# Optimization experiments

Hardware: AMD Instinct MI355X
Metric: run time of the kernel (lower is better)

Reference implementation:

```python
import jax, jax.numpy as jnp
import numpy as np

# Config constants (match init_kwargs)
E = 32          # num_experts
K = 4           # num_experts_per_token
G = 4           # num_expert_group
TG = 2          # topk_group
H = 2048        # hidden_size
F = 1024        # moe_intermediate_size
FS = 2048       # shared expert intermediate (moe_intermediate_size * num_shared_experts)
SCALE = 2.0     # routed_scaling_factor
B, S = 2, 1024
N = B * S
CAP = 2 * (N * K // E)


def setup_inputs() -> dict:
    key = jax.random.key(0)
    ks = jax.random.split(key, 9)
    w = 0.02  # init scale for weights
    return {
        "hidden_states": jax.random.normal(ks[0], (B, S, H), jnp.float32),
        "gate_w": jax.random.normal(ks[1], (E, H), jnp.float32) * w,
        "gate_bias": jax.random.normal(ks[2], (E,), jnp.float32) * w,
        "w1": jax.random.normal(ks[3], (E, H, F), jnp.float32) * w,
        "w2": jax.random.normal(ks[4], (E, F, H), jnp.float32) * w,
        "w3": jax.random.normal(ks[5], (E, H, F), jnp.float32) * w,
        "shared_gate": jax.random.normal(ks[6], (H, FS), jnp.float32) * w,
        "shared_up": jax.random.normal(ks[7], (H, FS), jnp.float32) * w,
        "shared_down": jax.random.normal(ks[8], (FS, H), jnp.float32) * w,
    }


def _gate(x, gate_w, gate_bias):
    # x: [N, H] -> (topk_idx [N,K] int32, topk_w [N,K] f32)
    logits = x @ gate_w.T                       # [N, E]
    scores = jax.nn.sigmoid(logits)
    sc = scores + gate_bias                     # scores_for_choice
    n = x.shape[0]
    grp = sc.reshape(n, G, E // G)
    group_scores = jax.lax.top_k(grp, 2)[0].sum(-1)          # [N, G]
    _, gidx = jax.lax.top_k(group_scores, TG)                # [N, TG]
    gmask = jnp.zeros((n, G), sc.dtype).at[jnp.arange(n)[:, None], gidx].set(1.0)
    smask = jnp.repeat(gmask, E // G, axis=1)                # [N, E]
    tmp = jnp.where(smask > 0, sc, 0.0)
    _, topk_idx = jax.lax.top_k(tmp, K)                      # [N, K]
    topk_w = jnp.take_along_axis(scores, topk_idx, axis=1)
    topk_w = topk_w / (topk_w.sum(-1, keepdims=True) + 1e-20)  # renormalize (K>1)
    return topk_idx, topk_w * SCALE


def _moe(x, topk_idx, topk_w, w1, w2, w3):
    # Capacity-based dispatch -> grouped SwiGLU GEMMs -> weighted combine.
    n = x.shape[0]
    flat_e = topk_idx.reshape(-1)                            # [N*K]
    oh = jax.nn.one_hot(flat_e, E, dtype=jnp.int32)
    pos = (jnp.cumsum(oh, axis=0) * oh).sum(-1) - 1          # slot within expert
    keep = pos < CAP
    slot = jnp.where(keep, pos, CAP)                         # CAP -> dropped via mode='drop'
    x_rep = jnp.repeat(x, K, axis=0)                         # [N*K, H]
    buf = jnp.zeros((E, CAP, H), x.dtype).at[flat_e, slot].set(x_rep, mode='drop')
    h = jax.nn.silu(jnp.einsum('ech,ehf->ecf', buf, w1)) * jnp.einsum('ech,ehf->ecf', buf, w3)
    ob = jnp.einsum('ecf,efh->ech', h, w2)                   # [E, CAP, H]
    y = ob[flat_e, jnp.minimum(slot, CAP - 1)]               # [N*K, H]
    y = jnp.where(keep[:, None], y, 0.0)
    return (y.reshape(n, K, H) * topk_w[:, :, None]).sum(1)  # [N, H]


def reference(hidden_states, gate_w, gate_bias, w1, w2, w3, shared_gate, shared_up, shared_down):
    b, s, h = hidden_states.shape
    x = hidden_states.reshape(-1, h)
    topk_idx, topk_w = _gate(x, gate_w, gate_bias)
    out = _moe(x, topk_idx, topk_w, w1, w2, w3)
    shared = (jax.nn.silu(x @ shared_gate) * (x @ shared_up)) @ shared_down
    return (out + shared).reshape(b, s, h)
```

## Files before the change

### kernel.cpp

```cpp
#include <hip/hip_runtime.h>
#include <stdint.h>
#include <math.h>

#define NTOK 2048
#define HDIM 2048
#define FDIM 1024
#define NEXP 32
#define TOPK 4
#define NGRP 4
#define CAP  512

typedef _Float16 f16;
typedef _Float16 half8 __attribute__((ext_vector_type(8)));
typedef float f32x4 __attribute__((ext_vector_type(4)));

__device__ __forceinline__ int swz3(int r) { return (r ^ (r >> 2)) & 3; }

__global__ __launch_bounds__(256) void convert_kernel(const float* __restrict__ x,
                                                      f16* __restrict__ xbt) {
  int i = blockIdx.x * 256 + threadIdx.x;
  int r = i >> 8;
  int c8 = (i & 255) << 3;
  const float* p = x + (size_t)r * HDIM + c8;
  f32x4 a = *(const f32x4*)p;
  f32x4 b = *(const f32x4*)(p + 4);
  half8 v;
  v[0] = (f16)a[0]; v[1] = (f16)a[1]; v[2] = (f16)a[2]; v[3] = (f16)a[3];
  v[4] = (f16)b[0]; v[5] = (f16)b[1]; v[6] = (f16)b[2]; v[7] = (f16)b[3];
  int t = c8 >> 5;
  *(half8*)((char*)xbt + (size_t)t * 131072 + r * 64 + (c8 & 31) * 2) = v;
}

__global__ __launch_bounds__(256) void gate_kernel(const float* __restrict__ x,
                                                   const float* __restrict__ gw,
                                                   const float* __restrict__ gb,
                                                   int* __restrict__ tidx,
                                                   float* __restrict__ tw) {
  int t = blockIdx.x;
  int tid = threadIdx.x;
  int e = tid >> 3, p = tid & 7;
  const f32x4* xr = (const f32x4*)(x + (size_t)t * HDIM);
  const f32x4* wr = (const f32x4*)(gw + (size_t)e * HDIM);
  float s = 0.f;
  for (int c = 0; c < 64; c++) {
    f32x4 a = xr[p + c * 8], w = wr[p + c * 8];
    s += a[0] * w[0] + a[1] * w[1] + a[2] * w[2] + a[3] * w[3];
  }
  s += __shfl_down(s, 4, 8);
  s += __shfl_down(s, 2, 8);
  s += __shfl_down(s, 1, 8);
  __shared__ float lg[NEXP];
  if (p == 0) lg[e] = s;
  __syncthreads();
  if (tid == 0) {
    float sc[NEXP], scb[NEXP];
    for (int i = 0; i < NEXP; i++) {
      sc[i] = 1.f / (1.f + expf(-lg[i]));
      scb[i] = sc[i] + gb[i];
    }
    float gs[NGRP];
    for (int g = 0; g < NGRP; g++) {
      float m1 = -1e30f, m2 = -1e30f;
      for (int j = 0; j < 8; j++) {
        float v = scb[g * 8 + j];
        if (v > m1) { m2 = m1; m1 = v; }
        else if (v > m2) m2 = v;
      }
      gs[g] = m1 + m2;
    }
    int g1 = 0; float bv = gs[0];
    for (int g = 1; g < NGRP; g++) if (gs[g] > bv) { bv = gs[g]; g1 = g; }
    int g2 = -1; bv = -1e30f;
    for (int g = 0; g < NGRP; g++) if (g != g1 && gs[g] > bv) { bv = gs[g]; g2 = g; }
    float cand[NEXP];
    for (int i = 0; i < NEXP; i++) {
      int g = i >> 3;
      cand[i] = (g == g1 || g == g2) ? scb[i] : 0.0f;
    }
    int isel[TOPK]; float wsel[TOPK]; float wsum = 0.f;
    bool used[NEXP] = {};
    for (int k = 0; k < TOPK; k++) {
      int best = 0; float bw = -1e30f;
      for (int i = 0; i < NEXP; i++)
        if (!used[i] && cand[i] > bw) { bw = cand[i]; best = i; }
      used[best] = true;
      isel[k] = best;
      wsel[k] = sc[best];
      wsum += wsel[k];
    }
    float inv = 2.0f / (wsum + 1e-20f);
    for (int k = 0; k < TOPK; k++) {
      tidx[t * TOPK + k] = isel[k];
      tw[t * TOPK + k] = wsel[k] * inv;
    }
  }
}

__global__ __launch_bounds__(256) void dispatch_kernel(const int* __restrict__ tidx,
                                                       const float* __restrict__ tw,
                                                       int* __restrict__ tok,
                                                       float* __restrict__ wt,
                                                       int* __restrict__ cnt) {
  int e = blockIdx.x, tid = threadIdx.x, wv = tid >> 6, lane = tid & 63;
  __shared__ int wsum[4];
  __shared__ int sbase;
  if (tid == 0) sbase = 0;
  __syncthreads();
  for (int c = 0; c < (NTOK * TOPK) / 256; c++) {
    int i = c * 256 + tid;
    int fe = tidx[i];
    bool flag = (fe == e);
    unsigned long long b = __ballot(flag ? 1 : 0);
    int lr = __popcll(b & ((1ull << lane) - 1ull));
    if (lane == 0) wsum[wv] = __popcll(b);
    __syncthreads();
    int off = 0;
    for (int w2 = 0; w2 < wv; w2++) off += wsum[w2];
    int tot = wsum[0] + wsum[1] + wsum[2] + wsum[3];
    int base = sbase;
    if (flag) {
      int pos = base + off + lr;
      if (pos < CAP) {
        tok[e * CAP + pos] = i >> 2;
        wt[e * CAP + pos] = tw[i];
      }
    }
    __syncthreads();
    if (tid == 0) sbase = base + tot;
  }
  __syncthreads();
  if (tid == 0) cnt[e] = min(sbase, CAP);
}

__global__ __launch_bounds__(256) void gather_kernel(const f16* __restrict__ xbt,
                                                     const int* __restrict__ tok,
                                                     const int* __restrict__ cnt,
                                                     f16* __restrict__ xg) {
  int bid = blockIdx.x;
  int t = bid & 63, e = bid >> 6;
  int cn = cnt[e];
  int tid = threadIdx.x;
  char* dst = (char*)xg + (size_t)e * 2097152 + (size_t)t * 32768;
  const char* srcb = (const char*)xbt + (size_t)t * 131072;
  for (int s = tid; s < CAP; s += 256) {
    uint4 v0 = {0,0,0,0}, v1 = {0,0,0,0}, v2 = {0,0,0,0}, v3 = {0,0,0,0};
    if (s < cn) {
      const uint4* sp = (const uint4*)(srcb + (size_t)tok[e * CAP + s] * 64);
      v0 = sp[0]; v1 = sp[1]; v2 = sp[2]; v3 = sp[3];
    }
    uint4* dp = (uint4*)(dst + s * 64);
    dp[0] = v0; dp[1] = v1; dp[2] = v2; dp[3] = v3;
  }
}

template<int MODE>
__global__ __launch_bounds__(256, (MODE == 1) ? 3 : ((MODE == 3) ? 4 : 2))
void gemm_kernel(const f16* __restrict__ Ag, const float* __restrict__ B0g,
                 const float* __restrict__ B1g, void* __restrict__ outp,
                 const int* __restrict__ tokL, const float* __restrict__ wtL,
                 const int* __restrict__ cntP) {
  constexpr int BM = (MODE == 0 || MODE == 2) ? 512 : 256;
  constexpr int BN = (MODE == 2) ? 64 : 32;
  constexpr bool DUAL = (MODE <= 1);
  constexpr int MF = BM / 64;
  constexpr int NF = BN / 16;
  constexpr int KD = (MODE == 2) ? 1024 : 2048;
  constexpr int NK = KD / 32;
  constexpr int ND = (MODE == 0) ? 1024 : 2048;
  constexpr int TS = (MODE == 0 || MODE == 2) ? 32768 : 131072;
  constexpr int BSZ = (DUAL ? 2 : 1) * BN * 64;

  int bid = blockIdx.x;
  int tid = threadIdx.x, lane = tid & 63, wv = tid >> 6;
  int e = 0, m0 = 0, n0 = 0;
  if constexpr (MODE == 0 || MODE == 2) {
    e = (bid & 7) + ((bid >> 3) >> 5) * 8;
    n0 = ((bid >> 3) & 31) * BN;
  } else {
    n0 = ((bid & 7) * 8 + ((bid >> 3) & 7)) * 32;
    m0 = ((bid >> 3) >> 3) * 256;
  }

  const char* Abase = (const char*)Ag;
  const float* B0 = B0g;
  const float* B1 = B1g;
  const int* tokp = tokL;
  const float* wtp = wtL;
  int Mcur = 0;
  if constexpr (MODE == 0 || MODE == 2) {
    Mcur = cntP[e];
    Abase += (size_t)e * ((MODE == 0) ? 2097152 : 1048576);
    B0 += (size_t)e * KD * ND;
    if constexpr (MODE == 0) B1 += (size_t)e * KD * ND;
    tokp += e * CAP;
    wtp += e * CAP;
  }

  __shared__ __align__(16) char bs[2 * BSZ];

  int kb = tid >> 3;
  int nbL = (tid & 7) * (BN / 8);

  unsigned voff[MF];
#pragma unroll
  for (int mf = 0; mf < MF; mf++) {
    int row = ((MODE == 0 || MODE == 2) ? (wv * (BM / 4)) : (m0 + wv * 64)) + mf * 16 + (lane & 15);
    voff[mf] = row * 64 + ((lane >> 4) << 4);
  }

  f32x4 acc0[MF][NF];
  f32x4 acc1[DUAL ? MF : 1][DUAL ? NF : 1];
#pragma unroll
  for (int mf = 0; mf < MF; mf++)
#pragma unroll
    for (int nf = 0; nf < NF; nf++) acc0[mf][nf] = (f32x4){0.f, 0.f, 0.f, 0.f};
  if constexpr (DUAL) {
#pragma unroll
    for (int mf = 0; mf < MF; mf++)
#pragma unroll
      for (int nf = 0; nf < NF; nf++) acc1[mf][nf] = (f32x4){0.f, 0.f, 0.f, 0.f};
  }

  half8 af[MF];
  half8 bf0[NF];
  half8 bf1[DUAL ? NF : 1];
  f32x4 bE0, bE1, bO0, bO1;

  auto loadB = [&](int t, f32x4& X, f32x4& Y) {
    const float* s = B0 + (size_t)(t * 32 + kb) * ND + n0 + nbL;
    X = *(const f32x4*)s;
    if constexpr (DUAL) {
      Y = *(const f32x4*)(B1 + (size_t)(t * 32 + kb) * ND + n0 + nbL);
    } else if constexpr (MODE == 2) {
      Y = *(const f32x4*)(s + 4);
    }
  };
  auto writeB = [&](const f32x4& X, const f32x4& Y, int par) {
    char* base = bs + par * BSZ;
#pragma unroll
    for (int q = 0; q < 4; q++) {
      int n = nbL + q;
      int off = n * 64 + (((kb >> 3) ^ swz3(n)) << 4) + (kb & 7) * 2;
      *(f16*)(base + off) = (f16)X[q];
      if constexpr (DUAL) {
        *(f16*)(base + BN * 64 + off) = (f16)Y[q];
      } else if constexpr (MODE == 2) {
        int n2 = n + 4;
        int off2 = n2 * 64 + (((kb >> 3) ^ swz3(n2)) << 4) + (kb & 7) * 2;
        *(f16*)(base + off2) = (f16)Y[q];
      }
    }
  };
  auto bfread = [&](int par) {
#pragma unroll
    for (int nf = 0; nf < NF; nf++) {
      int n = nf * 16 + (lane & 15);
      int off = par * BSZ + n * 64 + (((lane >> 4) ^ swz3(n)) << 4);
      bf0[nf] = *(const half8*)(bs + off);
      if constexpr (DUAL) bf1[nf] = *(const half8*)(bs + BN * 64 + off);
    }
  };
  auto loadAf = [&](int t) {
#pragma unroll
    for (int mf = 0; mf < MF; mf++)
      af[mf] = *(const half8*)(Abase + (size_t)t * TS + voff[mf]);
  };
  auto domfma = [&]() {
#pragma unroll
    for (int mf = 0; mf < MF; mf++)
#pragma unroll
      for (int nf = 0; nf < NF; nf++) {
        acc0[mf][nf] = __builtin_amdgcn_mfma_f32_16x16x32_f16(af[mf], bf0[nf], acc0[mf][nf], 0, 0, 0);
        if constexpr (DUAL)
          acc1[mf][nf] = __builtin_amdgcn_mfma_f32_16x16x32_f16(af[mf], bf1[nf], acc1[mf][nf], 0, 0, 0);
      }
  };

  loadB(0, bE0, bE1);
  loadB(1, bO0, bO1);
  loadAf(0);
  writeB(bE0, bE1, 0);
  asm volatile("s_waitcnt lgkmcnt(0)" ::: "memory");
  __builtin_amdgcn_s_barrier();

  for (int t = 0; t < NK; t += 2) {
    bfread(0);
    writeB(bO0, bO1, 1);
    if (t + 2 < NK) loadB(t + 2, bE0, bE1);
    domfma();
    loadAf(t + 1 < NK ? t + 1 : t);
    asm volatile("s_waitcnt lgkmcnt(0)" ::: "memory");
    __builtin_amdgcn_s_barrier();
    bfread(1);
    if (t + 2 < NK) writeB(bE0, bE1, 0);
    if (t + 3 < NK) loadB(t + 3, bO0, bO1);
    domfma();
    if (t + 2 < NK) {
      loadAf(t + 2);
      asm volatile("s_waitcnt lgkmcnt(0)" ::: "memory");
      __builtin_amdgcn_s_barrier();
    }
  }

  int koff = (lane >> 4) << 2;
  if constexpr (MODE == 0) {
    char* Hb = (char*)outp + (size_t)e * 1048576;
#pragma unroll
    for (int mf = 0; mf < MF; mf++)
#pragma unroll
      for (int j = 0; j < 4; j++) {
        int slot = wv * 128 + mf * 16 + koff + j;
#pragma unroll
        for (int nf = 0; nf < NF; nf++) {
          int col = n0 + nf * 16 + (lane & 15);
          float g = acc0[mf][nf][j], u = acc1[mf][nf][j];
          float val = g / (1.f + expf(-g)) * u;
          *(f16*)(Hb + (size_t)(col >> 5) * 32768 + slot * 64 + (col & 31) * 2) = (f16)val;
        }
      }
  } else if constexpr (MODE == 1) {
    char* Hb = (char*)outp;
#pragma unroll
    for (int mf = 0; mf < MF; mf++)
#pragma unroll
      for (int j = 0; j < 4; j++) {
        int row = m0 + wv * 64 + mf * 16 + koff + j;
#pragma unroll
        for (int nf = 0; nf < NF; nf++) {
          int col = n0 + nf * 16 + (lane & 15);
          float g = acc0[mf][nf][j], u = acc1[mf][nf][j];
          float val = g / (1.f + expf(-g)) * u;
          *(f16*)(Hb + (size_t)(col >> 5) * 131072 + row * 64 + (col & 31) * 2) = (f16)val;
        }
      }
  } else if constexpr (MODE == 2) {
    float* Of = (float*)outp;
#pragma unroll
    for (int mf = 0; mf < MF; mf++)
#pragma unroll
      for (int j = 0; j < 4; j++) {
        int slot = wv * 128 + mf * 16 + koff + j;
        if (slot < Mcur) {
          int tk = tokp[slot];
          float w = wtp[slot];
#pragma unroll
          for (int nf = 0; nf < NF; nf++) {
            int col = n0 + nf * 16 + (lane & 15);
            atomicAdd(Of + (size_t)tk * HDIM + col, acc0[mf][nf][j] * w);
          }
        }
      }
  } else {
    float* Of = (float*)outp;
#pragma unroll
    for (int mf = 0; mf < MF; mf++)
#pragma unroll
      for (int j = 0; j < 4; j++) {
        int row = m0 + wv * 64 + mf * 16 + koff + j;
#pragma unroll
        for (int nf = 0; nf < NF; nf++) {
          int col = n0 + nf * 16 + (lane & 15);
          Of[(size_t)row * HDIM + col] = acc0[mf][nf][j];
        }
      }
  }
}

extern "C" void kernel_launch(void* const* d_in, const int* in_sizes, int n_in,
                              void* d_out, int out_size, void* d_ws, size_t ws_size,
                              hipStream_t stream) {
  const float* x  = (const float*)d_in[0];
  const float* gw = (const float*)d_in[1];
  const float* gb = (const float*)d_in[2];
  const float* w1 = (const float*)d_in[3];
  const float* w2 = (const float*)d_in[4];
  const float* w3 = (const float*)d_in[5];
  const float* sg = (const float*)d_in[6];
  const float* su = (const float*)d_in[7];
  const float* sd = (const float*)d_in[8];
  float* out = (float*)d_out;
  char* ws = (char*)d_ws;

  f16*   xbt = (f16*)(ws);
  f16*   hs  = (f16*)(ws + 8388608);
  f16*   hbuf= (f16*)(ws + 16777216);
  f16*   xg  = (f16*)(ws + 50331648);
  int*   tok = (int*)(ws + 117440512);
  float* wt  = (float*)(ws + 117506048);
  int*   tidx= (int*)(ws + 117571584);
  float* tw  = (float*)(ws + 117604352);
  int*   cnt = (int*)(ws + 117637120);

  convert_kernel<<<2048, 256, 0, stream>>>(x, xbt);
  gate_kernel<<<2048, 256, 0, stream>>>(x, gw, gb, tidx, tw);
  dispatch_kernel<<<32, 256, 0, stream>>>(tidx, tw, tok, wt, cnt);
  gather_kernel<<<2048, 256, 0, stream>>>(xbt, tok, cnt, xg);

  gemm_kernel<0><<<1024, 256, 0, stream>>>(xg, w1, w3, hbuf, tok, wt, cnt);
  gemm_kernel<1><<<512, 256, 0, stream>>>(xbt, sg, su, hs, nullptr, nullptr, nullptr);
  gemm_kernel<3><<<512, 256, 0, stream>>>(hs, sd, nullptr, out, nullptr, nullptr, nullptr);
  gemm_kernel<2><<<1024, 256, 0, stream>>>(hbuf, w2, nullptr, out, tok, wt, cnt);
}
```

Before: 564.6 us.

## Load fp32 weights straight into MFMA B fragments, drop LDS staging

Each lane now loads B weights from global memory directly into registers, in the layout the MFMA fragment needs, and converts them to fp16 in registers. This removes the shared-memory staging, swizzle and barriers. Routed-expert blocks now skip waves whose rows are past the expert's token count. Tiling changes to BN=32 with one expert per block-index low bits, the mode-2 grid doubles, and the launch-bounds occupancy hints change. In exchange there are scalar, strided global loads that are less coalesced (16 columns across lanes, 8 rows per lane), and each wave re-reads B with no reuse across waves.

New measurement: 758.0 us. 34.2% more time.

```diff
diff --git a/kernel.cpp b/kernel.cpp
--- a/kernel.cpp
+++ b/kernel.cpp
@@ -13,8 +13,6 @@
 typedef _Float16 f16;
 typedef _Float16 half8 __attribute__((ext_vector_type(8)));
 typedef float f32x4 __attribute__((ext_vector_type(4)));
-
-__device__ __forceinline__ int swz3(int r) { return (r ^ (r >> 2)) & 3; }
 
 __global__ __launch_bounds__(256) void convert_kernel(const float* __restrict__ x,
                                                       f16* __restrict__ xbt) {
@@ -154,153 +152,125 @@
 }
 
 template<int MODE>
-__global__ __launch_bounds__(256, (MODE == 1) ? 3 : ((MODE == 3) ? 4 : 2))
+__global__ __launch_bounds__(256, (MODE <= 1) ? 2 : 3)
 void gemm_kernel(const f16* __restrict__ Ag, const float* __restrict__ B0g,
                  const float* __restrict__ B1g, void* __restrict__ outp,
                  const int* __restrict__ tokL, const float* __restrict__ wtL,
                  const int* __restrict__ cntP) {
-  constexpr int BM = (MODE == 0 || MODE == 2) ? 512 : 256;
-  constexpr int BN = (MODE == 2) ? 64 : 32;
   constexpr bool DUAL = (MODE <= 1);
-  constexpr int MF = BM / 64;
-  constexpr int NF = BN / 16;
+  constexpr bool ROUTED = (MODE == 0 || MODE == 2);
+  constexpr int WM = ROUTED ? 128 : 64;
+  constexpr int MF = WM / 16;
+  constexpr int NF = 2;
   constexpr int KD = (MODE == 2) ? 1024 : 2048;
   constexpr int NK = KD / 32;
   constexpr int ND = (MODE == 0) ? 1024 : 2048;
-  constexpr int TS = (MODE == 0 || MODE == 2) ? 32768 : 131072;
-  constexpr int BSZ = (DUAL ? 2 : 1) * BN * 64;
+  constexpr size_t TS = ROUTED ? 32768 : 131072;
 
   int bid = blockIdx.x;
   int tid = threadIdx.x, lane = tid & 63, wv = tid >> 6;
+
   int e = 0, m0 = 0, n0 = 0;
-  if constexpr (MODE == 0 || MODE == 2) {
-    e = (bid & 7) + ((bid >> 3) >> 5) * 8;
-    n0 = ((bid >> 3) & 31) * BN;
+  if constexpr (ROUTED) {
+    e = bid & 31;
+    n0 = (bid >> 5) * 32;
   } else {
-    n0 = ((bid & 7) * 8 + ((bid >> 3) & 7)) * 32;
-    m0 = ((bid >> 3) >> 3) * 256;
-  }
-
-  const char* Abase = (const char*)Ag;
+    m0 = (bid & 7) * 256;
+    n0 = (bid >> 3) * 32;
+  }
+
+  const char* Ab = (const char*)Ag;
   const float* B0 = B0g;
   const float* B1 = B1g;
-  const int* tokp = tokL;
-  const float* wtp = wtL;
-  int Mcur = 0;
-  if constexpr (MODE == 0 || MODE == 2) {
+  int Mcur = NTOK;
+  if constexpr (ROUTED) {
     Mcur = cntP[e];
-    Abase += (size_t)e * ((MODE == 0) ? 2097152 : 1048576);
-    B0 += (size_t)e * KD * ND;
-    if constexpr (MODE == 0) B1 += (size_t)e * KD * ND;
-    tokp += e * CAP;
-    wtp += e * CAP;
-  }
-
-  __shared__ __align__(16) char bs[2 * BSZ];
-
-  int kb = tid >> 3;
-  int nbL = (tid & 7) * (BN / 8);
-
-  unsigned voff[MF];
+    int Mpad = (Mcur + 127) & ~127;
+    if (wv * 128 >= Mpad) return;
+    Ab += (size_t)e * ((MODE == 0) ? 2097152 : 1048576);
+    B0 += (size_t)e * ((size_t)KD * ND);
+    if constexpr (DUAL) B1 += (size_t)e * ((size_t)KD * ND);
+  }
+
+  unsigned aoff[MF];
 #pragma unroll
   for (int mf = 0; mf < MF; mf++) {
-    int row = ((MODE == 0 || MODE == 2) ? (wv * (BM / 4)) : (m0 + wv * 64)) + mf * 16 + (lane & 15);
-    voff[mf] = row * 64 + ((lane >> 4) << 4);
-  }
-
+    int row = (ROUTED ? wv * WM : m0 + wv * WM) + mf * 16 + (lane & 15);
+    aoff[mf] = row * 64 + ((lane >> 4) << 4);
+  }
+
+  int q8 = (lane >> 4) * 8;
+  int nc = n0 + (lane & 15);
+
+  float bst0[NF][8];
+  float bst1[DUAL ? NF : 1][8];
+  half8 bc0[NF];
+  half8 bc1[DUAL ? NF : 1];
+  half8 afA[MF], afB[MF];
   f32x4 acc0[MF][NF];
   f32x4 acc1[DUAL ? MF : 1][DUAL ? NF : 1];
 #pragma unroll
   for (int mf = 0; mf < MF; mf++)
 #pragma unroll
-    for (int nf = 0; nf < NF; nf++) acc0[mf][nf] = (f32x4){0.f, 0.f, 0.f, 0.f};
+    for (int f = 0; f < NF; f++) acc0[mf][f] = (f32x4){0.f, 0.f, 0.f, 0.f};
   if constexpr (DUAL) {
 #pragma unroll
     for (int mf = 0; mf < MF; mf++)
 #pragma unroll
-      for (int nf = 0; nf < NF; nf++) acc1[mf][nf] = (f32x4){0.f, 0.f, 0.f, 0.f};
-  }
-
-  half8 af[MF];
-  half8 bf0[NF];
-  half8 bf1[DUAL ? NF : 1];
-  f32x4 bE0, bE1, bO0, bO1;
-
-  auto loadB = [&](int t, f32x4& X, f32x4& Y) {
-    const float* s = B0 + (size_t)(t * 32 + kb) * ND + n0 + nbL;
-    X = *(const f32x4*)s;
-    if constexpr (DUAL) {
-      Y = *(const f32x4*)(B1 + (size_t)(t * 32 + kb) * ND + n0 + nbL);
-    } else if constexpr (MODE == 2) {
-      Y = *(const f32x4*)(s + 4);
+      for (int f = 0; f < NF; f++) acc1[mf][f] = (f32x4){0.f, 0.f, 0.f, 0.f};
+  }
+
+  auto loadB = [&](int t) {
+#pragma unroll
+    for (int i = 0; i < 8; i++) {
+      size_t ro = (size_t)(t * 32 + q8 + i) * ND + nc;
+      bst0[0][i] = B0[ro];
+      bst0[1][i] = B0[ro + 16];
+      if constexpr (DUAL) {
+        bst1[0][i] = B1[ro];
+        bst1[1][i] = B1[ro + 16];
+      }
     }
   };
-  auto writeB = [&](const f32x4& X, const f32x4& Y, int par) {
-    char* base = bs + par * BSZ;
-#pragma unroll
-    for (int q = 0; q < 4; q++) {
-      int n = nbL + q;
-      int off = n * 64 + (((kb >> 3) ^ swz3(n)) << 4) + (kb & 7) * 2;
-      *(f16*)(base + off) = (f16)X[q];
-      if constexpr (DUAL) {
-        *(f16*)(base + BN * 64 + off) = (f16)Y[q];
-      } else if constexpr (MODE == 2) {
-        int n2 = n + 4;
-        int off2 = n2 * 64 + (((kb >> 3) ^ swz3(n2)) << 4) + (kb & 7) * 2;
-        *(f16*)(base + off2) = (f16)Y[q];
-      }
-    }
+  auto cvtB = [&]() {
+#pragma unroll
+    for (int f = 0; f < NF; f++)
+#pragma unroll
+      for (int i = 0; i < 8; i++) {
+        bc0[f][i] = (f16)bst0[f][i];
+        if constexpr (DUAL) bc1[f][i] = (f16)bst1[f][i];
+      }
   };
-  auto bfread = [&](int par) {
-#pragma unroll
-    for (int nf = 0; nf < NF; nf++) {
-      int n = nf * 16 + (lane & 15);
-      int off = par * BSZ + n * 64 + (((lane >> 4) ^ swz3(n)) << 4);
-      bf0[nf] = *(const half8*)(bs + off);
-      if constexpr (DUAL) bf1[nf] = *(const half8*)(bs + BN * 64 + off);
-    }
-  };
-  auto loadAf = [&](int t) {
-#pragma unroll
-    for (int mf = 0; mf < MF; mf++)
-      af[mf] = *(const half8*)(Abase + (size_t)t * TS + voff[mf]);
-  };
-  auto domfma = [&]() {
-#pragma unroll
-    for (int mf = 0; mf < MF; mf++)
-#pragma unroll
-      for (int nf = 0; nf < NF; nf++) {
-        acc0[mf][nf] = __builtin_amdgcn_mfma_f32_16x16x32_f16(af[mf], bf0[nf], acc0[mf][nf], 0, 0, 0);
-        if constexpr (DUAL)
-          acc1[mf][nf] = __builtin_amdgcn_mfma_f32_16x16x32_f16(af[mf], bf1[nf], acc1[mf][nf], 0, 0, 0);
-      }
-  };
-
-  loadB(0, bE0, bE1);
-  loadB(1, bO0, bO1);
-  loadAf(0);
-  writeB(bE0, bE1, 0);
-  asm volatile("s_waitcnt lgkmcnt(0)" ::: "memory");
-  __builtin_amdgcn_s_barrier();
-
+
+#define LOADAF(t, AF) { \
+  _Pragma("unroll") \
+  for (int mf = 0; mf < MF; mf++) \
+    AF[mf] = *(const half8*)(Ab + (size_t)(t) * TS + aoff[mf]); }
+
+#define DOMFMA(AF) { \
+  _Pragma("unroll") \
+  for (int mf = 0; mf < MF; mf++) { \
+    _Pragma("unroll") \
+    for (int f = 0; f < NF; f++) { \
+      acc0[mf][f] = __builtin_amdgcn_mfma_f32_16x16x32_f16(AF[mf], bc0[f], acc0[mf][f], 0, 0, 0); \
+      if constexpr (DUAL) \
+        acc1[mf][f] = __builtin_amdgcn_mfma_f32_16x16x32_f16(AF[mf], bc1[f], acc1[mf][f], 0, 0, 0); \
+    } } }
+
+  loadB(0);
+  LOADAF(0, afA)
   for (int t = 0; t < NK; t += 2) {
-    bfread(0);
-    writeB(bO0, bO1, 1);
-    if (t + 2 < NK) loadB(t + 2, bE0, bE1);
-    domfma();
-    loadAf(t + 1 < NK ? t + 1 : t);
-    asm volatile("s_waitcnt lgkmcnt(0)" ::: "memory");
-    __builtin_amdgcn_s_barrier();
-    bfread(1);
-    if (t + 2 < NK) writeB(bE0, bE1, 0);
-    if (t + 3 < NK) loadB(t + 3, bO0, bO1);
-    domfma();
-    if (t + 2 < NK) {
-      loadAf(t + 2);
-      asm volatile("s_waitcnt lgkmcnt(0)" ::: "memory");
-      __builtin_amdgcn_s_barrier();
-    }
-  }
+    cvtB();
+    loadB(t + 1);
+    DOMFMA(afA)
+    LOADAF(t + 1, afB)
+    cvtB();
+    if (t + 2 < NK) loadB(t + 2);
+    DOMFMA(afB)
+    if (t + 2 < NK) LOADAF(t + 2, afA)
+  }
+#undef LOADAF
+#undef DOMFMA
 
   int koff = (lane >> 4) << 2;
   if constexpr (MODE == 0) {
@@ -311,9 +281,9 @@
       for (int j = 0; j < 4; j++) {
         int slot = wv * 128 + mf * 16 + koff + j;
 #pragma unroll
-        for (int nf = 0; nf < NF; nf++) {
-          int col = n0 + nf * 16 + (lane & 15);
-          float g = acc0[mf][nf][j], u = acc1[mf][nf][j];
+        for (int f = 0; f < NF; f++) {
+          int col = n0 + f * 16 + (lane & 15);
+          float g = acc0[mf][f][j], u = acc1[mf][f][j];
           float val = g / (1.f + expf(-g)) * u;
           *(f16*)(Hb + (size_t)(col >> 5) * 32768 + slot * 64 + (col & 31) * 2) = (f16)val;
         }
@@ -326,15 +296,17 @@
       for (int j = 0; j < 4; j++) {
         int row = m0 + wv * 64 + mf * 16 + koff + j;
 #pragma unroll
-        for (int nf = 0; nf < NF; nf++) {
-          int col = n0 + nf * 16 + (lane & 15);
-          float g = acc0[mf][nf][j], u = acc1[mf][nf][j];
+        for (int f = 0; f < NF; f++) {
+          int col = n0 + f * 16 + (lane & 15);
+          float g = acc0[mf][f][j], u = acc1[mf][f][j];
           float val = g / (1.f + expf(-g)) * u;
           *(f16*)(Hb + (size_t)(col >> 5) * 131072 + row * 64 + (col & 31) * 2) = (f16)val;
         }
       }
   } else if constexpr (MODE == 2) {
     float* Of = (float*)outp;
+    const int* tokp = tokL + e * CAP;
+    const float* wtp = wtL + e * CAP;
 #pragma unroll
     for (int mf = 0; mf < MF; mf++)
 #pragma unroll
@@ -344,9 +316,9 @@
           int tk = tokp[slot];
           float w = wtp[slot];
 #pragma unroll
-          for (int nf = 0; nf < NF; nf++) {
-            int col = n0 + nf * 16 + (lane & 15);
-            atomicAdd(Of + (size_t)tk * HDIM + col, acc0[mf][nf][j] * w);
+          for (int f = 0; f < NF; f++) {
+            int col = n0 + f * 16 + (lane & 15);
+            atomicAdd(Of + (size_t)tk * HDIM + col, acc0[mf][f][j] * w);
           }
         }
       }
@@ -358,9 +330,9 @@
       for (int j = 0; j < 4; j++) {
         int row = m0 + wv * 64 + mf * 16 + koff + j;
 #pragma unroll
-        for (int nf = 0; nf < NF; nf++) {
-          int col = n0 + nf * 16 + (lane & 15);
-          Of[(size_t)row * HDIM + col] = acc0[mf][nf][j];
+        for (int f = 0; f < NF; f++) {
+          int col = n0 + f * 16 + (lane & 15);
+          Of[(size_t)row * HDIM + col] = acc0[mf][f][j];
         }
       }
   }
@@ -399,5 +371,5 @@
   gemm_kernel<0><<<1024, 256, 0, stream>>>(xg, w1, w3, hbuf, tok, wt, cnt);
   gemm_kernel<1><<<512, 256, 0, stream>>>(xbt, sg, su, hs, nullptr, nullptr, nullptr);
   gemm_kernel<3><<<512, 256, 0, stream>>>(hs, sd, nullptr, out, nullptr, nullptr, nullptr);
-  gemm_kernel<2><<<1024, 256, 0, stream>>>(hbuf, w2, nullptr, out, tok, wt, cnt);
-}
+  gemm_kernel<2><<<2048, 256, 0, stream>>>(hbuf, w2, nullptr, out, tok, wt, cnt);
+}
```

## Fuse routed and shared expert GEMMs into combined up and down launches

Applied to the files above, without the earlier changes.

The fp16 conversion of x now happens inside the gate kernel, so x is read once by one kernel instead of two. The gather now copies only occupied capacity slots and no longer zero-fills padding. The routed and shared up-projection GEMMs run as one launch, and the two down-projection GEMMs run as another, so the two expert paths can overlap on the device. Because both down GEMMs now add into the same output, the output is cleared with a memset and the shared path switches to atomic adds. The costs are extra atomic traffic on the output and lower allowed occupancy for the shared GEMM variants, since their launch bounds drop to 2 per CU.

Result: faster. 545.4 us (-3.4%).

```diff
diff --git a/kernel.cpp b/kernel.cpp
--- a/kernel.cpp
+++ b/kernel.cpp
@@ -14,28 +14,14 @@
 typedef _Float16 half8 __attribute__((ext_vector_type(8)));
 typedef float f32x4 __attribute__((ext_vector_type(4)));
 
-__device__ __forceinline__ int swz3(int r) { return (r ^ (r >> 2)) & 3; }
-
-__global__ __launch_bounds__(256) void convert_kernel(const float* __restrict__ x,
-                                                      f16* __restrict__ xbt) {
-  int i = blockIdx.x * 256 + threadIdx.x;
-  int r = i >> 8;
-  int c8 = (i & 255) << 3;
-  const float* p = x + (size_t)r * HDIM + c8;
-  f32x4 a = *(const f32x4*)p;
-  f32x4 b = *(const f32x4*)(p + 4);
-  half8 v;
-  v[0] = (f16)a[0]; v[1] = (f16)a[1]; v[2] = (f16)a[2]; v[3] = (f16)a[3];
-  v[4] = (f16)b[0]; v[5] = (f16)b[1]; v[6] = (f16)b[2]; v[7] = (f16)b[3];
-  int t = c8 >> 5;
-  *(half8*)((char*)xbt + (size_t)t * 131072 + r * 64 + (c8 & 31) * 2) = v;
-}
-
-__global__ __launch_bounds__(256) void gate_kernel(const float* __restrict__ x,
-                                                   const float* __restrict__ gw,
-                                                   const float* __restrict__ gb,
-                                                   int* __restrict__ tidx,
-                                                   float* __restrict__ tw) {
+__device__ __forceinline__ int swz3(int n) { return (n ^ (n >> 2)) & 3; }
+
+__global__ __launch_bounds__(256) void gateconv_kernel(const float* __restrict__ x,
+                                                       const float* __restrict__ gw,
+                                                       const float* __restrict__ gb,
+                                                       int* __restrict__ tidx,
+                                                       float* __restrict__ tw,
+                                                       f16* __restrict__ xbt) {
   int t = blockIdx.x;
   int tid = threadIdx.x;
   int e = tid >> 3, p = tid & 7;
@@ -51,6 +37,18 @@
   s += __shfl_down(s, 1, 8);
   __shared__ float lg[NEXP];
   if (p == 0) lg[e] = s;
+
+  {
+    int c8 = tid * 8;
+    const float* pp = x + (size_t)t * HDIM + c8;
+    f32x4 a = *(const f32x4*)pp;
+    f32x4 b = *(const f32x4*)(pp + 4);
+    half8 v;
+    v[0] = (f16)a[0]; v[1] = (f16)a[1]; v[2] = (f16)a[2]; v[3] = (f16)a[3];
+    v[4] = (f16)b[0]; v[5] = (f16)b[1]; v[6] = (f16)b[2]; v[7] = (f16)b[3];
+    *(half8*)((char*)xbt + (size_t)(c8 >> 5) * 131072 + t * 64 + (c8 & 31) * 2) = v;
+  }
+
   __syncthreads();
   if (tid == 0) {
     float sc[NEXP], scb[NEXP];
@@ -142,23 +140,19 @@
   int tid = threadIdx.x;
   char* dst = (char*)xg + (size_t)e * 2097152 + (size_t)t * 32768;
   const char* srcb = (const char*)xbt + (size_t)t * 131072;
-  for (int s = tid; s < CAP; s += 256) {
-    uint4 v0 = {0,0,0,0}, v1 = {0,0,0,0}, v2 = {0,0,0,0}, v3 = {0,0,0,0};
-    if (s < cn) {
-      const uint4* sp = (const uint4*)(srcb + (size_t)tok[e * CAP + s] * 64);
-      v0 = sp[0]; v1 = sp[1]; v2 = sp[2]; v3 = sp[3];
-    }
+  for (int s = tid; s < cn; s += 256) {
+    const uint4* sp = (const uint4*)(srcb + (size_t)tok[e * CAP + s] * 64);
+    uint4 v0 = sp[0], v1 = sp[1], v2 = sp[2], v3 = sp[3];
     uint4* dp = (uint4*)(dst + s * 64);
     dp[0] = v0; dp[1] = v1; dp[2] = v2; dp[3] = v3;
   }
 }
 
 template<int MODE>
-__global__ __launch_bounds__(256, (MODE == 1) ? 3 : ((MODE == 3) ? 4 : 2))
-void gemm_kernel(const f16* __restrict__ Ag, const float* __restrict__ B0g,
-                 const float* __restrict__ B1g, void* __restrict__ outp,
-                 const int* __restrict__ tokL, const float* __restrict__ wtL,
-                 const int* __restrict__ cntP) {
+__device__ void gemm_body(int bid, const f16* __restrict__ Ag, const float* __restrict__ B0g,
+                          const float* __restrict__ B1g, void* __restrict__ outp,
+                          const int* __restrict__ tokL, const float* __restrict__ wtL,
+                          const int* __restrict__ cntP, char* bs) {
   constexpr int BM = (MODE == 0 || MODE == 2) ? 512 : 256;
   constexpr int BN = (MODE == 2) ? 64 : 32;
   constexpr bool DUAL = (MODE <= 1);
@@ -167,10 +161,9 @@
   constexpr int KD = (MODE == 2) ? 1024 : 2048;
   constexpr int NK = KD / 32;
   constexpr int ND = (MODE == 0) ? 1024 : 2048;
-  constexpr int TS = (MODE == 0 || MODE == 2) ? 32768 : 131072;
+  constexpr size_t TS = (MODE == 0 || MODE == 2) ? 32768 : 131072;
   constexpr int BSZ = (DUAL ? 2 : 1) * BN * 64;
 
-  int bid = blockIdx.x;
   int tid = threadIdx.x, lane = tid & 63, wv = tid >> 6;
   int e = 0, m0 = 0, n0 = 0;
   if constexpr (MODE == 0 || MODE == 2) {
@@ -181,22 +174,16 @@
     m0 = ((bid >> 3) >> 3) * 256;
   }
 
-  const char* Abase = (const char*)Ag;
+  const char* Ab = (const char*)Ag;
   const float* B0 = B0g;
   const float* B1 = B1g;
-  const int* tokp = tokL;
-  const float* wtp = wtL;
   int Mcur = 0;
   if constexpr (MODE == 0 || MODE == 2) {
     Mcur = cntP[e];
-    Abase += (size_t)e * ((MODE == 0) ? 2097152 : 1048576);
-    B0 += (size_t)e * KD * ND;
-    if constexpr (MODE == 0) B1 += (size_t)e * KD * ND;
-    tokp += e * CAP;
-    wtp += e * CAP;
-  }
-
-  __shared__ __align__(16) char bs[2 * BSZ];
+    Ab += (size_t)e * ((MODE == 0) ? 2097152 : 1048576);
+    B0 += (size_t)e * ((size_t)KD * ND);
+    if constexpr (MODE == 0) B1 += (size_t)e * ((size_t)KD * ND);
+  }
 
   int kb = tid >> 3;
   int nbL = (tid & 7) * (BN / 8);
@@ -263,7 +250,7 @@
   auto loadAf = [&](int t) {
 #pragma unroll
     for (int mf = 0; mf < MF; mf++)
-      af[mf] = *(const half8*)(Abase + (size_t)t * TS + voff[mf]);
+      af[mf] = *(const half8*)(Ab + (size_t)t * TS + voff[mf]);
   };
   auto domfma = [&]() {
 #pragma unroll
@@ -310,12 +297,14 @@
 #pragma unroll
       for (int j = 0; j < 4; j++) {
         int slot = wv * 128 + mf * 16 + koff + j;
-#pragma unroll
-        for (int nf = 0; nf < NF; nf++) {
-          int col = n0 + nf * 16 + (lane & 15);
-          float g = acc0[mf][nf][j], u = acc1[mf][nf][j];
-          float val = g / (1.f + expf(-g)) * u;
-          *(f16*)(Hb + (size_t)(col >> 5) * 32768 + slot * 64 + (col & 31) * 2) = (f16)val;
+        if (slot < Mcur) {
+#pragma unroll
+          for (int nf = 0; nf < NF; nf++) {
+            int col = n0 + nf * 16 + (lane & 15);
+            float g = acc0[mf][nf][j], u = acc1[mf][nf][j];
+            float val = g / (1.f + expf(-g)) * u;
+            *(f16*)(Hb + (size_t)(col >> 5) * 32768 + slot * 64 + (col & 31) * 2) = (f16)val;
+          }
         }
       }
   } else if constexpr (MODE == 1) {
@@ -335,6 +324,8 @@
       }
   } else if constexpr (MODE == 2) {
     float* Of = (float*)outp;
+    const int* tokp = tokL + e * CAP;
+    const float* wtp = wtL + e * CAP;
 #pragma unroll
     for (int mf = 0; mf < MF; mf++)
 #pragma unroll
@@ -360,10 +351,32 @@
 #pragma unroll
         for (int nf = 0; nf < NF; nf++) {
           int col = n0 + nf * 16 + (lane & 15);
-          Of[(size_t)row * HDIM + col] = acc0[mf][nf][j];
+          atomicAdd(Of + (size_t)row * HDIM + col, acc0[mf][nf][j]);
         }
       }
   }
+}
+
+__global__ __launch_bounds__(256, 2) void fused_up_kernel(
+    const f16* __restrict__ xg, const f16* __restrict__ xbt,
+    const float* __restrict__ w1, const float* __restrict__ w3,
+    const float* __restrict__ sg, const float* __restrict__ su,
+    void* __restrict__ hbuf, void* __restrict__ hs, const int* __restrict__ cnt) {
+  __shared__ __align__(16) char bs[8192];
+  int bid = blockIdx.x;
+  if (bid < 1024) gemm_body<0>(bid, xg, w1, w3, hbuf, nullptr, nullptr, cnt, bs);
+  else            gemm_body<1>(bid - 1024, xbt, sg, su, hs, nullptr, nullptr, nullptr, bs);
+}
+
+__global__ __launch_bounds__(256, 2) void fused_down_kernel(
+    const f16* __restrict__ hbuf, const f16* __restrict__ hs,
+    const float* __restrict__ w2, const float* __restrict__ sd,
+    float* __restrict__ out, const int* __restrict__ tok,
+    const float* __restrict__ wt, const int* __restrict__ cnt) {
+  __shared__ __align__(16) char bs[8192];
+  int bid = blockIdx.x;
+  if (bid < 1024) gemm_body<2>(bid, hbuf, w2, nullptr, out, tok, wt, cnt, bs);
+  else            gemm_body<3>(bid - 1024, hs, sd, nullptr, out, nullptr, nullptr, nullptr, bs);
 }
 
 extern "C" void kernel_launch(void* const* d_in, const int* in_sizes, int n_in,
@@ -391,13 +404,12 @@
   float* tw  = (float*)(ws + 117604352);
   int*   cnt = (int*)(ws + 117637120);
 
-  convert_kernel<<<2048, 256, 0, stream>>>(x, xbt);
-  gate_kernel<<<2048, 256, 0, stream>>>(x, gw, gb, tidx, tw);
+  gateconv_kernel<<<2048, 256, 0, stream>>>(x, gw, gb, tidx, tw, xbt);
   dispatch_kernel<<<32, 256, 0, stream>>>(tidx, tw, tok, wt, cnt);
   gather_kernel<<<2048, 256, 0, stream>>>(xbt, tok, cnt, xg);
 
-  gemm_kernel<0><<<1024, 256, 0, stream>>>(xg, w1, w3, hbuf, tok, wt, cnt);
-  gemm_kernel<1><<<512, 256, 0, stream>>>(xbt, sg, su, hs, nullptr, nullptr, nullptr);
-  gemm_kernel<3><<<512, 256, 0, stream>>>(hs, sd, nullptr, out, nullptr, nullptr, nullptr);
-  gemm_kernel<2><<<1024, 256, 0, stream>>>(hbuf, w2, nullptr, out, tok, wt, cnt);
-}
+  fused_up_kernel<<<1536, 256, 0, stream>>>(xg, xbt, w1, w3, sg, su, hbuf, hs, cnt);
+
+  hipMemsetAsync(out, 0, (size_t)out_size * sizeof(float), stream);
+  fused_down_kernel<<<1536, 256, 0, stream>>>(hbuf, hs, w2, sd, out, tok, wt, cnt);
+}
```
